# Optimization experiments

Measured on AMD Instinct MI355X. Metric: run time of the kernel, lower is better.

Reference implementation:

```python
import jax, jax.numpy as jnp
import numpy as np

DIM_MODEL = 1024
NUM_HEADS = 16
DIM_HEAD = 64
B, S = 2, 2048


def setup_inputs() -> dict:
    key = jax.random.key(0)
    ks = jax.random.split(key, 10)
    scale = 1.0 / np.sqrt(DIM_MODEL)
    inp = {
        "x": jax.random.normal(ks[0], (B, S, DIM_MODEL), dtype=jnp.float32),
        "padding_mask": jax.random.randint(ks[1], (B, S), 0, 2, dtype=jnp.int32),
        "Wq": jax.random.normal(ks[2], (DIM_MODEL, DIM_MODEL), dtype=jnp.float32) * scale,
        "bq": jnp.zeros((DIM_MODEL,), dtype=jnp.float32),
        "Wk": jax.random.normal(ks[3], (DIM_MODEL, DIM_MODEL), dtype=jnp.float32) * scale,
        "bk": jnp.zeros((DIM_MODEL,), dtype=jnp.float32),
        "Wv": jax.random.normal(ks[4], (DIM_MODEL, DIM_MODEL), dtype=jnp.float32) * scale,
        "bv": jnp.zeros((DIM_MODEL,), dtype=jnp.float32),
        "Wo": jax.random.normal(ks[5], (DIM_MODEL, DIM_MODEL), dtype=jnp.float32) * scale,
        "bo": jnp.zeros((DIM_MODEL,), dtype=jnp.float32),
    }
    return inp


def reference(x, padding_mask, Wq, bq, Wk, bk, Wv, bv, Wo, bo):
    b, s, _ = x.shape
    dot_scale = jnp.sqrt(jnp.asarray(DIM_HEAD, dtype=x.dtype))
    # projections -> (b, h, s, d)
    q = (x @ Wq + bq).reshape(b, s, NUM_HEADS, DIM_HEAD).transpose(0, 2, 1, 3)
    k = (x @ Wk + bk).reshape(b, s, NUM_HEADS, DIM_HEAD).transpose(0, 2, 1, 3)
    v = (x @ Wv + bv).reshape(b, s, NUM_HEADS, DIM_HEAD).transpose(0, 2, 1, 3)
    # scores (b, h, s, s)
    scores = jnp.einsum("bhqd,bhkd->bhqk", q, k) / dot_scale
    mask = (padding_mask == 1)[:, None, None, :]  # (b,1,1,s) over key positions
    scores = jnp.where(mask, -jnp.inf, scores)
    attn = jax.nn.softmax(scores, axis=-1)
    out = jnp.einsum("bhqk,bhkd->bhqd", attn, v)
    out = out.transpose(0, 2, 1, 3).reshape(b, s, NUM_HEADS * DIM_HEAD)
    return out @ Wo + bo
```

## Files before the change

### kernel.cpp

```cpp
#include <hip/hip_runtime.h>
#include <hip/hip_bf16.h>
#include <stdint.h>
#include <math.h>

#define D_MODEL 1024
#define NHEAD   16
#define DHEAD   64
#define BATCH   2
#define SEQ     2048
#define M_TOK   (BATCH * SEQ)

#define QSCALE 0.18033688011112042f

typedef __attribute__((ext_vector_type(8))) short   short8;
typedef __attribute__((ext_vector_type(8))) __bf16  bf16x8;
typedef __attribute__((ext_vector_type(4))) float   f32x4;

__device__ inline short f2bf(float f) {
  unsigned int u = __builtin_bit_cast(unsigned int, f);
  unsigned int r = (u + 0x7FFFu + ((u >> 16) & 1u)) >> 16;
  return (short)(unsigned short)r;
}
__device__ inline short f2bf_fast(float f) {
  unsigned int u = __builtin_bit_cast(unsigned int, f);
  return (short)(unsigned short)((u + 0x8000u) >> 16);
}

__device__ inline void gl_lds16(const void* g, void* l) {
  __builtin_amdgcn_global_load_lds((__attribute__((address_space(1))) void*)(g),
                                   (__attribute__((address_space(3))) void*)(l),
                                   16, 0, 0);
}

__device__ inline bf16x8 lds_frag(const short* p) {
  return *(const bf16x8*)(p);
}
__device__ inline bf16x8 lds_frag64(const short* p) {
  union { bf16x8 v; short4 h[2]; } u;
  u.h[0] = *(const short4*)(p);
  u.h[1] = *(const short4*)(p + 4);
  return u.v;
}

__global__ __launch_bounds__(256) void prep(const float* __restrict__ x,
                                            short* __restrict__ xb,
                                            const float* __restrict__ w0,
                                            const float* __restrict__ w1,
                                            const float* __restrict__ w2,
                                            const float* __restrict__ w3,
                                            short* __restrict__ out) {
  const int t = threadIdx.x;
  if (blockIdx.z == 4) {
    size_t base = ((size_t)blockIdx.y * 16 + blockIdx.x) * 16384;
    const float* in = x + base;
    short* o = xb + base;
#pragma unroll
    for (int i = 0; i < 16; ++i) {
      f32x4 v = *(const f32x4*)(in + (size_t)t * 4 + i * 1024);
      short4 s4;
      s4.x = f2bf(v[0]); s4.y = f2bf(v[1]); s4.z = f2bf(v[2]); s4.w = f2bf(v[3]);
      *(short4*)(o + (size_t)t * 4 + i * 1024) = s4;
    }
    return;
  }
  __shared__ short tile[64][72];
  const float* W = blockIdx.z == 0 ? w0 : blockIdx.z == 1 ? w1 : blockIdx.z == 2 ? w2 : w3;
  short* O = out + (size_t)blockIdx.z * (D_MODEL * (size_t)D_MODEL);
  int n0 = blockIdx.x * 64, k0 = blockIdx.y * 64;
#pragma unroll
  for (int i = 0; i < 16; ++i) {
    int idx = t + 256 * i;
    int r = idx >> 6, c = idx & 63;
    tile[r][c] = f2bf(W[(size_t)(k0 + r) * D_MODEL + n0 + c]);
  }
  __syncthreads();
#pragma unroll
  for (int i = 0; i < 16; ++i) {
    int idx = t + 256 * i;
    int r = idx >> 6, c = idx & 63;
    O[(size_t)(n0 + r) * D_MODEL + k0 + c] = tile[c][r];
  }
}

template <bool OUTF32, bool VT, int TN>
__global__ __launch_bounds__(256) void gemm128(const short* __restrict__ A,
                                               const short* __restrict__ Bt_base,
                                               const float* __restrict__ b0,
                                               const float* __restrict__ b1,
                                               const float* __restrict__ b2,
                                               void* __restrict__ out_base,
                                               short* __restrict__ vt,
                                               const int* __restrict__ pm) {
  constexpr int NI = TN / 32;
  const int z = blockIdx.z;
  const short* Bt   = Bt_base + (size_t)z * (D_MODEL * (size_t)D_MODEL);
  const float* bias = (z == 0) ? b0 : (z == 1) ? b1 : b2;

  __shared__ short As[128 * 64];
  __shared__ short Bs[TN * 64];

  const int t = threadIdx.x;
  const int lane = t & 63;
  const int wid = t >> 6;
  const int wm = (wid >> 1) * 64, wn = (wid & 1) * (TN / 2);
  const int m0 = blockIdx.x * 128, n0 = blockIdx.y * TN;
  const int cl = lane & 15, q = lane >> 4;
  const int sw = cl & 7;

  f32x4 acc[4][NI];
#pragma unroll
  for (int i = 0; i < 4; ++i)
#pragma unroll
    for (int j = 0; j < NI; ++j) acc[i][j] = 0.0f;

  for (int k0 = 0; k0 < D_MODEL; k0 += 64) {
    __syncthreads();
#pragma unroll
    for (int i = 0; i < 4; ++i) {
      int c = t + 256 * i;
      int row = c >> 3, cp = c & 7;
      int col = ((cp ^ (row & 7)) * 8);
      gl_lds16(A + (size_t)(m0 + row) * D_MODEL + k0 + col, (void*)(As + c * 8));
    }
#pragma unroll
    for (int i = 0; i < NI; ++i) {
      int c = t + 256 * i;
      int row = c >> 3, cp = c & 7;
      int col = ((cp ^ (row & 7)) * 8);
      gl_lds16(Bt + (size_t)(n0 + row) * D_MODEL + k0 + col, (void*)(Bs + c * 8));
    }
    __syncthreads();

    bf16x8 af[4][2], bfr[NI][2];
#pragma unroll
    for (int mi = 0; mi < 4; ++mi) {
      af[mi][0] = lds_frag(As + (wm + mi * 16 + cl) * 64 + (q ^ sw) * 8);
      af[mi][1] = lds_frag(As + (wm + mi * 16 + cl) * 64 + ((4 + q) ^ sw) * 8);
    }
#pragma unroll
    for (int ni = 0; ni < NI; ++ni) {
      bfr[ni][0] = lds_frag(Bs + (wn + ni * 16 + cl) * 64 + (q ^ sw) * 8);
      bfr[ni][1] = lds_frag(Bs + (wn + ni * 16 + cl) * 64 + ((4 + q) ^ sw) * 8);
    }
#pragma unroll
    for (int mi = 0; mi < 4; ++mi)
#pragma unroll
      for (int ni = 0; ni < NI; ++ni) {
        acc[mi][ni] = __builtin_amdgcn_mfma_f32_16x16x32_bf16(af[mi][0], bfr[ni][0], acc[mi][ni], 0, 0, 0);
        acc[mi][ni] = __builtin_amdgcn_mfma_f32_16x16x32_bf16(af[mi][1], bfr[ni][1], acc[mi][ni], 0, 0, 0);
      }
  }

  const float oscale = (VT && z == 0) ? QSCALE : 1.0f;
  int4 mm[4];
  if (VT && z == 2) {
#pragma unroll
    for (int mi = 0; mi < 4; ++mi) {
      int rbase = m0 + wm + mi * 16 + q * 4;
      mm[mi] = *(const int4*)(pm + (size_t)(rbase >> 11) * SEQ + (rbase & (SEQ - 1)));
    }
  }
#pragma unroll
  for (int ni = 0; ni < NI; ++ni) {
    int col = n0 + wn + ni * 16 + cl;
    float bv = bias[col];
#pragma unroll
    for (int mi = 0; mi < 4; ++mi) {
      int rbase = m0 + wm + mi * 16 + q * 4;
      if (VT && z == 2) {
        short4 o4;
        o4.x = (mm[mi].x == 1) ? (short)0 : f2bf_fast(acc[mi][ni][0] + bv);
        o4.y = (mm[mi].y == 1) ? (short)0 : f2bf_fast(acc[mi][ni][1] + bv);
        o4.z = (mm[mi].z == 1) ? (short)0 : f2bf_fast(acc[mi][ni][2] + bv);
        o4.w = (mm[mi].w == 1) ? (short)0 : f2bf_fast(acc[mi][ni][3] + bv);
        int btok = rbase >> 11;
        int s    = rbase & (SEQ - 1);
        *(short4*)(vt + (size_t)btok * ((size_t)D_MODEL * SEQ) + (size_t)col * SEQ + s) = o4;
      } else {
#pragma unroll
        for (int r = 0; r < 4; ++r) {
          float v = (acc[mi][ni][r] + bv) * oscale;
          size_t idx = (size_t)(rbase + r) * D_MODEL + col;
          if (OUTF32) {
            ((float*)out_base)[idx] = v;
          } else {
            short* out = (short*)out_base + (size_t)z * ((size_t)M_TOK * D_MODEL);
            out[idx] = f2bf_fast(v);
          }
        }
      }
    }
  }
}

__global__ __launch_bounds__(512) void attn_flash(const short* __restrict__ Q,
                                                  const short* __restrict__ K,
                                                  const short* __restrict__ Vt,
                                                  const int*   __restrict__ mask,
                                                  short* __restrict__ ctx) {
  const int qb = blockIdx.x;
  const int h  = blockIdx.y;
  const int b  = blockIdx.z;

  __shared__ __align__(16) short QPs[17408];
  __shared__ __align__(16) short Ks[2 * 64 * 64];
  __shared__ __align__(16) short Vts[2 * 64 * 64];
  __shared__ __align__(16) short Us[2 * 64];

  const int t = threadIdx.x;
  const int lane = t & 63;
  const int wid = t >> 6;
  const int wg  = wid >> 1;
  const int kvh = wid & 1;
  const int cl = lane & 15, q = lane >> 4;
  const int sw = cl & 7;

  const size_t rowQ0 = (size_t)b * SEQ + (size_t)qb * 128;
  const size_t rowK0 = (size_t)b * SEQ;
  const size_t vbase = ((size_t)b * D_MODEL + h * DHEAD) * SEQ;

#pragma unroll
  for (int i = 0; i < 2; ++i) {
    int c = t + 512 * i;
    int row = c >> 3, cp = c & 7;
    gl_lds16(Q + (rowQ0 + row) * D_MODEL + h * DHEAD + ((cp ^ (row & 7)) * 8),
             (void*)(QPs + c * 8));
  }
  __syncthreads();

  bf16x8 qf[2][2];
#pragma unroll
  for (int rb = 0; rb < 2; ++rb) {
    int row = wg * 32 + rb * 16 + cl;
    qf[rb][0] = lds_frag(QPs + row * 64 + (q ^ sw) * 8);
    qf[rb][1] = lds_frag(QPs + row * 64 + ((4 + q) ^ sw) * 8);
  }
  short* Psw = QPs + wid * (32 * 68);
  const short* Kp = Ks  + kvh * 4096;
  const short* Vp = Vts + kvh * 4096;
  const short* Up = Us  + kvh * 64;

  f32x4 lacc[2], oacc[2][4];
#pragma unroll
  for (int rb = 0; rb < 2; ++rb) {
    lacc[rb] = 0.0f;
#pragma unroll
    for (int dj = 0; dj < 4; ++dj) oacc[rb][dj] = 0.0f;
  }

  for (int s0 = 0; s0 < 1024; s0 += 64) {
    __syncthreads();

    {
      int row = t >> 3, cp = t & 7;
      int col = (cp ^ (row & 7)) * 8;
      gl_lds16(K + (rowK0 + s0 + row) * D_MODEL + h * DHEAD + col,
               (void*)(Ks + t * 8));
      gl_lds16(K + (rowK0 + 1024 + s0 + row) * D_MODEL + h * DHEAD + col,
               (void*)(Ks + 4096 + t * 8));
      gl_lds16(Vt + vbase + (size_t)row * SEQ + s0 + col,
               (void*)(Vts + t * 8));
      gl_lds16(Vt + vbase + (size_t)row * SEQ + 1024 + s0 + col,
               (void*)(Vts + 4096 + t * 8));
    }
    if (t < 128)
      Us[t] = (mask[(size_t)b * SEQ + (t >> 6) * 1024 + s0 + (t & 63)] == 1)
                  ? (short)0 : (short)0x3F80;
    __syncthreads();

    f32x4 s[2][4];
#pragma unroll
    for (int j = 0; j < 4; ++j) {
      bf16x8 kf0 = lds_frag(Kp + (j * 16 + cl) * 64 + (q ^ sw) * 8);
      bf16x8 kf1 = lds_frag(Kp + (j * 16 + cl) * 64 + ((4 + q) ^ sw) * 8);
#pragma unroll
      for (int rb = 0; rb < 2; ++rb) {
        f32x4 sa = 0.0f;
        sa = __builtin_amdgcn_mfma_f32_16x16x32_bf16(qf[rb][0], kf0, sa, 0, 0, 0);
        sa = __builtin_amdgcn_mfma_f32_16x16x32_bf16(qf[rb][1], kf1, sa, 0, 0, 0);
        s[rb][j] = sa;
      }
    }

#pragma unroll
    for (int rb = 0; rb < 2; ++rb)
#pragma unroll
      for (int j = 0; j < 4; ++j)
#pragma unroll
        for (int r = 0; r < 4; ++r)
          Psw[(rb * 16 + q * 4 + r) * 68 + j * 16 + cl] = f2bf_fast(exp2f(s[rb][j][r]));

    asm volatile("" ::: "memory");

    bf16x8 pf[2][2];
#pragma unroll
    for (int rb = 0; rb < 2; ++rb) {
      pf[rb][0] = lds_frag64(Psw + (rb * 16 + cl) * 68 + q * 8);
      pf[rb][1] = lds_frag64(Psw + (rb * 16 + cl) * 68 + 32 + q * 8);
    }
    bf16x8 uf0 = lds_frag(Up + q * 8);
    bf16x8 uf1 = lds_frag(Up + 32 + q * 8);
#pragma unroll
    for (int dj = 0; dj < 4; ++dj) {
      bf16x8 vf0 = lds_frag(Vp + (dj * 16 + cl) * 64 + (q ^ sw) * 8);
      bf16x8 vf1 = lds_frag(Vp + (dj * 16 + cl) * 64 + ((4 + q) ^ sw) * 8);
#pragma unroll
      for (int rb = 0; rb < 2; ++rb) {
        oacc[rb][dj] = __builtin_amdgcn_mfma_f32_16x16x32_bf16(pf[rb][0], vf0, oacc[rb][dj], 0, 0, 0);
        oacc[rb][dj] = __builtin_amdgcn_mfma_f32_16x16x32_bf16(pf[rb][1], vf1, oacc[rb][dj], 0, 0, 0);
      }
    }
#pragma unroll
    for (int rb = 0; rb < 2; ++rb) {
      lacc[rb] = __builtin_amdgcn_mfma_f32_16x16x32_bf16(pf[rb][0], uf0, lacc[rb], 0, 0, 0);
      lacc[rb] = __builtin_amdgcn_mfma_f32_16x16x32_bf16(pf[rb][1], uf1, lacc[rb], 0, 0, 0);
    }
  }

  __syncthreads();
  float* redO = (float*)QPs;
  float* redL = (float*)Ks;
  const int rbase = (wg * 64 + lane) * 32;
  const int lbase = (wg * 64 + lane) * 8;
  if (kvh) {
#pragma unroll
    for (int rb = 0; rb < 2; ++rb) {
#pragma unroll
      for (int dj = 0; dj < 4; ++dj) {
        int qi = (rb * 4 + dj) ^ (lane & 7);
        *(f32x4*)(redO + rbase + qi * 4) = oacc[rb][dj];
      }
      *(f32x4*)(redL + lbase + rb * 4) = lacc[rb];
    }
  }
  __syncthreads();
  if (kvh) return;
#pragma unroll
  for (int rb = 0; rb < 2; ++rb) {
    lacc[rb] += *(const f32x4*)(redL + lbase + rb * 4);
#pragma unroll
    for (int dj = 0; dj < 4; ++dj) {
      int qi = (rb * 4 + dj) ^ (lane & 7);
      oacc[rb][dj] += *(const f32x4*)(redO + rbase + qi * 4);
    }
  }

#pragma unroll
  for (int rb = 0; rb < 2; ++rb)
#pragma unroll
    for (int dj = 0; dj < 4; ++dj)
#pragma unroll
      for (int r = 0; r < 4; ++r) {
        float lv = lacc[rb][r];
        float o = (lv > 0.0f) ? oacc[rb][dj][r] / lv : 0.0f;
        size_t row = rowQ0 + wg * 32 + rb * 16 + q * 4 + r;
        ctx[row * D_MODEL + h * DHEAD + dj * 16 + cl] = f2bf(o);
      }
}

extern "C" void kernel_launch(void* const* d_in, const int* in_sizes, int n_in,
                              void* d_out, int out_size, void* d_ws, size_t ws_size,
                              hipStream_t stream) {
  (void)in_sizes; (void)n_in; (void)out_size; (void)ws_size;

  const float* x  = (const float*)d_in[0];
  const int*   pm = (const int*)  d_in[1];
  const float* Wq = (const float*)d_in[2];
  const float* bq = (const float*)d_in[3];
  const float* Wk = (const float*)d_in[4];
  const float* bk = (const float*)d_in[5];
  const float* Wv = (const float*)d_in[6];
  const float* bv = (const float*)d_in[7];
  const float* Wo = (const float*)d_in[8];
  const float* bo = (const float*)d_in[9];

  const size_t WMAT = (size_t)D_MODEL * D_MODEL;
  const size_t TOKD = (size_t)M_TOK * D_MODEL;

  short* base = (short*)d_ws;
  short* Wt = base;
  short* xb = base + 4 * WMAT;
  short* Qw = xb + TOKD;
  short* Kw = Qw + TOKD;
  short* Vtw = Kw + TOKD;
  short* Cw = Vtw + TOKD;

  prep<<<dim3(16, 16, 5), 256, 0, stream>>>(x, xb, Wq, Wk, Wv, Wo, Wt);
  gemm128<false, true, 128><<<dim3(M_TOK / 128, D_MODEL / 128, 3), 256, 0, stream>>>(
      xb, Wt, bq, bk, bv, Qw, Vtw, pm);
  attn_flash<<<dim3(SEQ / 128, NHEAD, BATCH), 512, 0, stream>>>(Qw, Kw, Vtw, pm, Cw);
  gemm128<true, false, 64><<<dim3(M_TOK / 128, D_MODEL / 64, 1), 256, 0, stream>>>(
      Cw, Wt + 3 * WMAT, bo, bo, bo, d_out, nullptr, nullptr);
}
```

Before: 214.4 us.

## Register-prefetch next K/V tile, preload full mask, use raw exp2 intrinsic

Replaces the synchronous global-to-LDS K/V loads with register prefetching. The next tile's K and V are loaded into registers while the current tile is being computed, then written to LDS at the start of the next iteration. The whole padding mask for the sequence is converted once into LDS up front, which removes the per-iteration mask load. exp2f is swapped for the hardware exp2 intrinsic. This costs more VGPRs and 4KB more LDS, which may reduce occupancy, and the intrinsic skips exp2f's denormal handling.

```diff
diff --git a/kernel.cpp b/kernel.cpp
--- a/kernel.cpp
+++ b/kernel.cpp
@@ -205,7 +205,7 @@
   __shared__ __align__(16) short QPs[17408];
   __shared__ __align__(16) short Ks[2 * 64 * 64];
   __shared__ __align__(16) short Vts[2 * 64 * 64];
-  __shared__ __align__(16) short Us[2 * 64];
+  __shared__ __align__(16) short Usall[SEQ];
 
   const int t = threadIdx.x;
   const int lane = t & 63;
@@ -219,6 +219,24 @@
   const size_t rowK0 = (size_t)b * SEQ;
   const size_t vbase = ((size_t)b * D_MODEL + h * DHEAD) * SEQ;
 
+  const int srow = t >> 3, scp = t & 7;
+  const int scol = (scp ^ (srow & 7)) * 8;
+  const short* Kg0 = K + (rowK0 + srow) * D_MODEL + h * DHEAD + scol;
+  const short* Kg1 = K + (rowK0 + 1024 + srow) * D_MODEL + h * DHEAD + scol;
+  const short* Vg0 = Vt + vbase + (size_t)srow * SEQ + scol;
+  const short* Vg1 = Vt + vbase + (size_t)srow * SEQ + 1024 + scol;
+
+  short8 gk0 = *(const short8*)(Kg0);
+  short8 gk1 = *(const short8*)(Kg1);
+  short8 gv0 = *(const short8*)(Vg0);
+  short8 gv1 = *(const short8*)(Vg1);
+
+#pragma unroll
+  for (int i = 0; i < 4; ++i) {
+    int idx = t + 512 * i;
+    Usall[idx] = (mask[(size_t)b * SEQ + idx] == 1) ? (short)0 : (short)0x3F80;
+  }
+
 #pragma unroll
   for (int i = 0; i < 2; ++i) {
     int c = t + 512 * i;
@@ -238,7 +256,6 @@
   short* Psw = QPs + wid * (32 * 68);
   const short* Kp = Ks  + kvh * 4096;
   const short* Vp = Vts + kvh * 4096;
-  const short* Up = Us  + kvh * 64;
 
   f32x4 lacc[2], oacc[2][4];
 #pragma unroll
@@ -251,22 +268,21 @@
   for (int s0 = 0; s0 < 1024; s0 += 64) {
     __syncthreads();
 
-    {
-      int row = t >> 3, cp = t & 7;
-      int col = (cp ^ (row & 7)) * 8;
-      gl_lds16(K + (rowK0 + s0 + row) * D_MODEL + h * DHEAD + col,
-               (void*)(Ks + t * 8));
-      gl_lds16(K + (rowK0 + 1024 + s0 + row) * D_MODEL + h * DHEAD + col,
-               (void*)(Ks + 4096 + t * 8));
-      gl_lds16(Vt + vbase + (size_t)row * SEQ + s0 + col,
-               (void*)(Vts + t * 8));
-      gl_lds16(Vt + vbase + (size_t)row * SEQ + 1024 + s0 + col,
-               (void*)(Vts + 4096 + t * 8));
-    }
-    if (t < 128)
-      Us[t] = (mask[(size_t)b * SEQ + (t >> 6) * 1024 + s0 + (t & 63)] == 1)
-                  ? (short)0 : (short)0x3F80;
+    *(short8*)(Ks  + t * 8)        = gk0;
+    *(short8*)(Ks  + 4096 + t * 8) = gk1;
+    *(short8*)(Vts + t * 8)        = gv0;
+    *(short8*)(Vts + 4096 + t * 8) = gv1;
     __syncthreads();
+
+    if (s0 + 64 < 1024) {
+      int sn = s0 + 64;
+      gk0 = *(const short8*)(Kg0 + (size_t)sn * D_MODEL);
+      gk1 = *(const short8*)(Kg1 + (size_t)sn * D_MODEL);
+      gv0 = *(const short8*)(Vg0 + sn);
+      gv1 = *(const short8*)(Vg1 + sn);
+    }
+
+    const short* Up = Usall + kvh * 1024 + s0;
 
     f32x4 s[2][4];
 #pragma unroll
@@ -288,7 +304,8 @@
       for (int j = 0; j < 4; ++j)
 #pragma unroll
         for (int r = 0; r < 4; ++r)
-          Psw[(rb * 16 + q * 4 + r) * 68 + j * 16 + cl] = f2bf_fast(exp2f(s[rb][j][r]));
+          Psw[(rb * 16 + q * 4 + r) * 68 + j * 16 + cl] =
+              f2bf_fast(__builtin_amdgcn_exp2f(s[rb][j][r]));
 
     asm volatile("" ::: "memory");
 
```

After: 209.5 us. -2.3%, faster.
